# Performance work log

Hardware: AMD Instinct MI355X
Metric: run time of the kernel (lower is better)

The kernel has to match this reference:

```python
import jax, jax.numpy as jnp
import numpy as np

NCHW = ('NCHW', 'OIHW', 'NCHW')


def _conv3x3_same(x, w, b):
    # ZeroPad2d(1) + 3x3 valid conv == 3x3 conv with padding 1
    y = jax.lax.conv_general_dilated(x, w, window_strides=(1, 1),
                                     padding=((1, 1), (1, 1)),
                                     dimension_numbers=NCHW)
    return y + b[None, :, None, None]


def _maxpool2(x):
    return jax.lax.reduce_window(x, -jnp.inf, jax.lax.max,
                                 (1, 1, 2, 2), (1, 1, 2, 2), 'VALID')


def setup_inputs() -> dict:
    key = jax.random.key(0)
    ks = jax.random.split(key, 12)
    B, T1, T2, R, D = 1, 512, 512, 9, 3840
    q = jax.random.normal(ks[0], (B, T1, R, D), jnp.float32)
    t = jax.random.normal(ks[1], (B, T2, R, D), jnp.float32)
    # ViSiL features are L2-normalized region descriptors -> sims in [-1,1]
    q = q / jnp.linalg.norm(q, axis=-1, keepdims=True)
    t = t / jnp.linalg.norm(t, axis=-1, keepdims=True)
    s = 0.05
    return {
        'query': q, 'target': t,
        'w1': jax.random.normal(ks[2], (32, 1, 3, 3), jnp.float32) * s,
        'b1': jax.random.normal(ks[3], (32,), jnp.float32) * s,
        'w2': jax.random.normal(ks[4], (64, 32, 3, 3), jnp.float32) * s,
        'b2': jax.random.normal(ks[5], (64,), jnp.float32) * s,
        'w3': jax.random.normal(ks[6], (128, 64, 3, 3), jnp.float32) * s,
        'b3': jax.random.normal(ks[7], (128,), jnp.float32) * s,
        'wf': jax.random.normal(ks[8], (1, 128, 1, 1), jnp.float32) * s,
        'bf': jax.random.normal(ks[9], (1,), jnp.float32) * s,
    }


def reference(query, target, w1, b1, w2, b2, w3, b3, wf, bf):
    # frame-to-frame: region-pair similarity [B,T1,O,P,T2]
    sim5 = jnp.einsum('biok,bjpk->biopj', query, target)
    # Chamfer (axes=[3,2]): max over target regions P, mean over query regions O
    f2f = jnp.mean(jnp.max(sim5, axis=3), axis=2)  # [B,T1,T2]
    # video comperator CNN
    x = f2f[:, None]                                 # [B,1,T1,T2]
    x = _maxpool2(jax.nn.relu(_conv3x3_same(x, w1, b1)))
    x = _maxpool2(jax.nn.relu(_conv3x3_same(x, w2, b2)))
    x = jax.nn.relu(_conv3x3_same(x, w3, b3))
    x = jax.lax.conv_general_dilated(x, wf, (1, 1), ((0, 0), (0, 0)),
                                     dimension_numbers=NCHW)
    x = x + bf[None, :, None, None]
    s = jnp.clip(x[:, 0], -1.0, 1.0)                 # Hardtanh, [B,H,W]
    # video-to-video Chamfer (axes=[2,1]): max over axis 2, mean over axis 1
    return jnp.mean(jnp.max(s, axis=2), axis=1)      # [B]
```

## Files before the change

kernel.cpp:

```cpp
#include <hip/hip_runtime.h>
#include <hip/hip_bf16.h>

typedef float f32x4 __attribute__((ext_vector_type(4)));

#define AS3 __attribute__((address_space(3)))
#define AS1 __attribute__((address_space(1)))

__global__ __launch_bounds__(256) void cvt_fp8_kernel(const float* __restrict__ src,
                                                      unsigned int* __restrict__ dst,
                                                      int n16) {
  int idx = blockIdx.x * 256 + threadIdx.x;
  if (idx >= n16) return;
  const float4* s4 = (const float4*)src;
  uint4 o;
  unsigned int* op = (unsigned int*)&o;
#pragma unroll
  for (int i = 0; i < 4; ++i) {
    float4 v = s4[idx * 4 + i];
    int w = 0;
    w = __builtin_amdgcn_cvt_pk_fp8_f32(v.x * 16.f, v.y * 16.f, w, false);
    w = __builtin_amdgcn_cvt_pk_fp8_f32(v.z * 16.f, v.w * 16.f, w, true);
    op[i] = w;
  }
  ((uint4*)dst)[idx] = o;
}

__global__ __launch_bounds__(768) void gemm_cmax_kernel(const unsigned char* __restrict__ qf8,
                                                        const unsigned char* __restrict__ tf8,
                                                        float* __restrict__ cmax) {
  __shared__ __align__(16) char smem[73728];
  const int tid  = threadIdx.x;
  const int wv   = tid >> 6;
  const int lane = tid & 63;
  const int quad = lane >> 4;
  const int l16  = lane & 15;
  const int wrow = wv >> 1, wcol = wv & 1;
  const int bi = blockIdx.y, bj = blockIdx.x;

  f32x4 acc[3][9];
#pragma unroll
  for (int a = 0; a < 3; ++a)
#pragma unroll
    for (int b = 0; b < 9; ++b) acc[a][b] = (f32x4){0.f, 0.f, 0.f, 0.f};

  const unsigned char* gptr[3];
#pragma unroll
  for (int r = 0; r < 3; ++r) {
    int c   = r * 768 + wv * 64 + lane;
    int mat = (c >= 1152);
    int cm  = c - mat * 1152;
    int row = cm >> 2, cl = cm & 3;
    int gch = cl ^ ((row >> 1) & 3);
    const unsigned char* base = mat ? (tf8 + (size_t)(bj * 288 + row) * 3840)
                                    : (qf8 + (size_t)(bi * 288 + row) * 3840);
    gptr[r] = base + gch * 16;
  }

  int buf = 0;
#pragma unroll
  for (int r = 0; r < 3; ++r)
    __builtin_amdgcn_global_load_lds((const AS1 void*)(gptr[r]),
                                     (AS3 void*)(smem + (r * 768 + wv * 64) * 16), 16, 0, 0);

  const int arow0 = wrow * 48 + l16;
  const int bcol0 = wcol * 144 + l16;

  for (int kt = 0; kt < 60; ++kt) {
    __syncthreads();
    if (kt < 59) {
      int nb = buf ^ 1;
#pragma unroll
      for (int r = 0; r < 3; ++r)
        __builtin_amdgcn_global_load_lds((const AS1 void*)(gptr[r] + (kt + 1) * 64),
                                         (AS3 void*)(smem + nb * 36864 + (r * 768 + wv * 64) * 16),
                                         16, 0, 0);
    }
    const char* A = smem + buf * 36864;
    const char* B = A + 18432;
#pragma unroll
    for (int ks = 0; ks < 2; ++ks) {
      long av[3];
#pragma unroll
      for (int sr = 0; sr < 3; ++sr) {
        int row = arow0 + sr * 16;
        int ch  = ((ks * 2 + (quad >> 1)) ^ ((row >> 1) & 3));
        av[sr] = *(const long*)(A + row * 64 + ch * 16 + (quad & 1) * 8);
      }
#pragma unroll
      for (int c = 0; c < 9; ++c) {
        int col = bcol0 + c * 16;
        int ch  = ((ks * 2 + (quad >> 1)) ^ ((col >> 1) & 3));
        long bv = *(const long*)(B + col * 64 + ch * 16 + (quad & 1) * 8);
        acc[0][c] = __builtin_amdgcn_mfma_f32_16x16x32_fp8_fp8(av[0], bv, acc[0][c], 0, 0, 0);
        acc[1][c] = __builtin_amdgcn_mfma_f32_16x16x32_fp8_fp8(av[1], bv, acc[1][c], 0, 0, 0);
        acc[2][c] = __builtin_amdgcn_mfma_f32_16x16x32_fp8_fp8(av[2], bv, acc[2][c], 0, 0, 0);
      }
    }
    buf ^= 1;
  }

  __syncthreads();
  float* scr = (float*)smem;
#pragma unroll
  for (int b = 0; b < 18; ++b) {
    const int bw = b / 3, bs = b - bw * 3;
    if (wrow == bw) {
#pragma unroll
      for (int c = 0; c < 9; ++c)
#pragma unroll
        for (int r = 0; r < 4; ++r)
          scr[(quad * 4 + r) * 288 + wcol * 144 + c * 16 + l16] = acc[bs][c][r] * (1.f / 256.f);
    }
    __syncthreads();
    if (tid < 512) {
      int row = tid >> 5, jg = tid & 31;
      const float* p = scr + row * 288 + jg * 9;
      float m = p[0];
#pragma unroll
      for (int k = 1; k < 9; ++k) m = fmaxf(m, p[k]);
      cmax[(size_t)(bi * 288 + b * 16 + row) * 512 + bj * 32 + jg] = m;
    }
    __syncthreads();
  }
}

__global__ __launch_bounds__(512) void mean9_kernel(const float* __restrict__ cmax,
                                                    float* __restrict__ f2f) {
  int i = blockIdx.x, j = threadIdx.x;
  float s = 0.f;
#pragma unroll
  for (int o = 0; o < 9; ++o) s += cmax[(size_t)(i * 9 + o) * 512 + j];
  f2f[i * 512 + j] = s * (1.f / 9.f);
}

__global__ __launch_bounds__(256) void conv1_kernel(const float* __restrict__ in,
                                                    const float* __restrict__ w1,
                                                    const float* __restrict__ b1,
                                                    float* __restrict__ out) {
  __shared__ float tile[34 * 36];
  __shared__ float wl[320];
  int t = blockIdx.x;
  int ty0 = (t >> 4) * 32, tx0 = (t & 15) * 32;
  int py = threadIdx.x >> 4, px = threadIdx.x & 15;

  for (int idx = threadIdx.x; idx < 320; idx += 256)
    wl[idx] = (idx < 288) ? w1[idx] : b1[idx - 288];
  for (int idx = threadIdx.x; idx < 34 * 34; idx += 256) {
    int r = idx / 34, c = idx % 34;
    int gy = ty0 + r - 1, gx = tx0 + c - 1;
    tile[r * 36 + c] = ((unsigned)gy < 512u && (unsigned)gx < 512u) ? in[gy * 512 + gx] : 0.f;
  }
  __syncthreads();

  float win[4][4];
#pragma unroll
  for (int r = 0; r < 4; ++r)
#pragma unroll
    for (int c = 0; c < 4; ++c)
      win[r][c] = tile[(2 * py + r) * 36 + 2 * px + c];

  int gy2 = (t >> 4) * 16 + py, gx2 = (t & 15) * 16 + px;
#pragma unroll 1
  for (int ch = 0; ch < 32; ++ch) {
    float w[9];
#pragma unroll
    for (int k = 0; k < 9; ++k) w[k] = wl[ch * 9 + k];
    float m = -INFINITY;
#pragma unroll
    for (int a = 0; a < 2; ++a)
#pragma unroll
      for (int b = 0; b < 2; ++b) {
        float s = 0.f;
#pragma unroll
        for (int ky = 0; ky < 3; ++ky)
#pragma unroll
          for (int kx = 0; kx < 3; ++kx) s += win[a + ky][b + kx] * w[ky * 3 + kx];
        m = fmaxf(m, s);
      }
    out[ch * 65536 + gy2 * 256 + gx2] = fmaxf(m + wl[288 + ch], 0.f);
  }
}

__global__ __launch_bounds__(256) void conv2_kernel(const float* __restrict__ in,
                                                    const float* __restrict__ w2,
                                                    const float* __restrict__ b2,
                                                    float* __restrict__ out) {
  __shared__ __align__(16) float wlds[32 * 8 * 12];
  __shared__ float tile[2][2][34 * 36];
  const int tid = threadIdx.x;
  int cog = blockIdx.x >> 6;
  int t   = blockIdx.x & 63;
  int ty0 = (t >> 3) * 32, tx0 = (t & 7) * 32;
  int py = tid >> 4, px = tid & 15;

  for (int idx = tid; idx < 2304; idx += 256) {
    int co = idx / 288, rem = idx % 288, ci = rem / 9, k = rem % 9;
    wlds[(ci * 8 + co) * 12 + k] = w2[((cog * 8 + co) * 32 + ci) * 9 + k];
  }
  for (int idx = tid; idx < 2312; idx += 256) {
    int pl = idx / 1156, rc = idx % 1156, r = rc / 34, c = rc % 34;
    int gy = ty0 + r - 1, gx = tx0 + c - 1;
    tile[0][pl][r * 36 + c] = ((unsigned)gy < 256u && (unsigned)gx < 256u)
                                  ? in[pl * 65536 + gy * 256 + gx] : 0.f;
  }
  __syncthreads();

  float acc[4][8];
#pragma unroll
  for (int p = 0; p < 4; ++p)
#pragma unroll
    for (int co = 0; co < 8; ++co) acc[p][co] = 0.f;

#pragma unroll 1
  for (int cb = 0; cb < 16; ++cb) {
    int buf = cb & 1;
    float pf[10];
    if (cb < 15) {
#pragma unroll
      for (int i = 0; i < 10; ++i) {
        int idx = tid + i * 256;
        float v = 0.f;
        if (idx < 2312) {
          int pl = idx / 1156, rc = idx % 1156, r = rc / 34, c = rc % 34;
          int gy = ty0 + r - 1, gx = tx0 + c - 1;
          if ((unsigned)gy < 256u && (unsigned)gx < 256u)
            v = in[((cb + 1) * 2 + pl) * 65536 + gy * 256 + gx];
        }
        pf[i] = v;
      }
    }
#pragma unroll
    for (int pl = 0; pl < 2; ++pl) {
      float win[4][4];
#pragma unroll
      for (int r = 0; r < 4; ++r) {
        float2 lo = *(const float2*)&tile[buf][pl][(2 * py + r) * 36 + 2 * px];
        float2 hi = *(const float2*)&tile[buf][pl][(2 * py + r) * 36 + 2 * px + 2];
        win[r][0] = lo.x; win[r][1] = lo.y; win[r][2] = hi.x; win[r][3] = hi.y;
      }
      int ci = cb * 2 + pl;
#pragma unroll
      for (int co = 0; co < 8; ++co) {
        const float* wp = &wlds[(ci * 8 + co) * 12];
        float4 w0 = *(const float4*)wp;
        float4 w1v = *(const float4*)(wp + 4);
        float w8 = wp[8];
        float w[9] = {w0.x, w0.y, w0.z, w0.w, w1v.x, w1v.y, w1v.z, w1v.w, w8};
#pragma unroll
        for (int a = 0; a < 2; ++a)
#pragma unroll
          for (int b = 0; b < 2; ++b) {
            float s = acc[a * 2 + b][co];
#pragma unroll
            for (int ky = 0; ky < 3; ++ky)
#pragma unroll
              for (int kx = 0; kx < 3; ++kx) s += win[a + ky][b + kx] * w[ky * 3 + kx];
            acc[a * 2 + b][co] = s;
          }
      }
    }
    if (cb < 15) {
#pragma unroll
      for (int i = 0; i < 10; ++i) {
        int idx = tid + i * 256;
        if (idx < 2312) {
          int pl = idx / 1156, rc = idx % 1156, r = rc / 34, c = rc % 34;
          tile[buf ^ 1][pl][r * 36 + c] = pf[i];
        }
      }
    }
    __syncthreads();
  }

  int gy2 = (t >> 3) * 16 + py, gx2 = (t & 7) * 16 + px;
#pragma unroll
  for (int co = 0; co < 8; ++co) {
    float m = fmaxf(fmaxf(acc[0][co], acc[1][co]), fmaxf(acc[2][co], acc[3][co]));
    out[(cog * 8 + co) * 16384 + gy2 * 128 + gx2] = fmaxf(m + b2[cog * 8 + co], 0.f);
  }
}

__global__ __launch_bounds__(256) void conv3_kernel(const float* __restrict__ in,
                                                    const float* __restrict__ w3,
                                                    const float* __restrict__ b3,
                                                    float* __restrict__ out) {
  __shared__ __align__(16) float wlds[64 * 8 * 12];
  __shared__ float tile[2][4][18 * 40];
  const int tid = threadIdx.x;
  int cog = blockIdx.x >> 5;
  int t   = blockIdx.x & 31;
  int ty0 = (t >> 2) * 16, tx0 = (t & 3) * 32;
  int py = tid >> 4, px = tid & 15;

  for (int idx = tid; idx < 4608; idx += 256) {
    int co = idx / 576, rem = idx % 576, ci = rem / 9, k = rem % 9;
    wlds[(ci * 8 + co) * 12 + k] = w3[((cog * 8 + co) * 64 + ci) * 9 + k];
  }
  for (int idx = tid; idx < 2448; idx += 256) {
    int pl = idx / 612, rc = idx % 612, r = rc / 34, c = rc % 34;
    int gy = ty0 + r - 1, gx = tx0 + c - 1;
    tile[0][pl][r * 40 + c] = ((unsigned)gy < 128u && (unsigned)gx < 128u)
                                  ? in[pl * 16384 + gy * 128 + gx] : 0.f;
  }
  __syncthreads();

  float acc[2][8];
#pragma unroll
  for (int p = 0; p < 2; ++p)
#pragma unroll
    for (int co = 0; co < 8; ++co) acc[p][co] = 0.f;

#pragma unroll 1
  for (int cb = 0; cb < 16; ++cb) {
    int buf = cb & 1;
    float pf[10];
    if (cb < 15) {
#pragma unroll
      for (int i = 0; i < 10; ++i) {
        int idx = tid + i * 256;
        float v = 0.f;
        if (idx < 2448) {
          int pl = idx / 612, rc = idx % 612, r = rc / 34, c = rc % 34;
          int gy = ty0 + r - 1, gx = tx0 + c - 1;
          if ((unsigned)gy < 128u && (unsigned)gx < 128u)
            v = in[((cb + 1) * 4 + pl) * 16384 + gy * 128 + gx];
        }
        pf[i] = v;
      }
    }
#pragma unroll
    for (int pl = 0; pl < 4; ++pl) {
      float win[3][6];
#pragma unroll
      for (int r = 0; r < 3; ++r) {
#pragma unroll
        for (int c = 0; c < 3; ++c) {
          win[r][c]     = tile[buf][pl][(py + r) * 40 + px + c];
          win[r][3 + c] = tile[buf][pl][(py + r) * 40 + px + 16 + c];
        }
      }
      int ci = cb * 4 + pl;
#pragma unroll
      for (int co = 0; co < 8; ++co) {
        const float* wp = &wlds[(ci * 8 + co) * 12];
        float4 w0 = *(const float4*)wp;
        float4 w1v = *(const float4*)(wp + 4);
        float w8 = wp[8];
        float w[9] = {w0.x, w0.y, w0.z, w0.w, w1v.x, w1v.y, w1v.z, w1v.w, w8};
        float s0 = acc[0][co], s1 = acc[1][co];
#pragma unroll
        for (int ky = 0; ky < 3; ++ky)
#pragma unroll
          for (int kx = 0; kx < 3; ++kx) {
            s0 += win[ky][kx] * w[ky * 3 + kx];
            s1 += win[ky][3 + kx] * w[ky * 3 + kx];
          }
        acc[0][co] = s0; acc[1][co] = s1;
      }
    }
    if (cb < 15) {
#pragma unroll
      for (int i = 0; i < 10; ++i) {
        int idx = tid + i * 256;
        if (idx < 2448) {
          int pl = idx / 612, rc = idx % 612, r = rc / 34, c = rc % 34;
          tile[buf ^ 1][pl][r * 40 + c] = pf[i];
        }
      }
    }
    __syncthreads();
  }

  int y = ty0 + py;
#pragma unroll
  for (int co = 0; co < 8; ++co) {
    float bias = b3[cog * 8 + co];
    out[(cog * 8 + co) * 16384 + y * 128 + tx0 + px]      = fmaxf(acc[0][co] + bias, 0.f);
    out[(cog * 8 + co) * 16384 + y * 128 + tx0 + px + 16] = fmaxf(acc[1][co] + bias, 0.f);
  }
}

__global__ __launch_bounds__(512) void convf_kernel(const float* __restrict__ in,
                                                    const float* __restrict__ wf,
                                                    const float* __restrict__ bfp,
                                                    float* __restrict__ rowm) {
  __shared__ float part[512];
  int y = blockIdx.x, tid = threadIdx.x;
  int pt = tid >> 7, x = tid & 127;
  float acc = 0.f;
  const float* ip = in + y * 128 + x;
  for (int ci = pt * 32; ci < pt * 32 + 32; ++ci) acc += ip[ci * 16384] * wf[ci];
  part[tid] = acc;
  __syncthreads();
  if (tid < 128) {
    float s = part[tid] + part[tid + 128] + part[tid + 256] + part[tid + 384] + bfp[0];
    part[tid] = fminf(fmaxf(s, -1.f), 1.f);
  }
  __syncthreads();
  if (tid < 64) {
    float m = fmaxf(part[tid], part[tid + 64]);
    for (int off = 32; off; off >>= 1) m = fmaxf(m, __shfl_down(m, off, 64));
    if (tid == 0) rowm[y] = m;
  }
}

__global__ __launch_bounds__(128) void final_kernel(const float* __restrict__ rowm,
                                                    float* __restrict__ out) {
  int x = threadIdx.x;
  float v = rowm[x];
  for (int off = 32; off; off >>= 1) v += __shfl_down(v, off, 64);
  __shared__ float red[2];
  if ((x & 63) == 0) red[x >> 6] = v;
  __syncthreads();
  if (x == 0) out[0] = (red[0] + red[1]) * (1.f / 128.f);
}

extern "C" void kernel_launch(void* const* d_in, const int* in_sizes, int n_in,
                              void* d_out, int out_size, void* d_ws, size_t ws_size,
                              hipStream_t stream) {
  const float* q  = (const float*)d_in[0];
  const float* t  = (const float*)d_in[1];
  const float* w1 = (const float*)d_in[2];
  const float* b1 = (const float*)d_in[3];
  const float* w2 = (const float*)d_in[4];
  const float* b2 = (const float*)d_in[5];
  const float* w3 = (const float*)d_in[6];
  const float* b3 = (const float*)d_in[7];
  const float* wf = (const float*)d_in[8];
  const float* bf = (const float*)d_in[9];
  float* out = (float*)d_out;
  char* ws = (char*)d_ws;

  unsigned char* qf8 = (unsigned char*)(ws + 0);
  unsigned char* tf8 = (unsigned char*)(ws + 17694720);
  float* cmax = (float*)(ws + 35389440);
  float* f2f  = (float*)(ws + 44826624);
  float* x1   = (float*)(ws + 45875200);
  float* x2b  = (float*)(ws + 54263808);
  float* x3   = (float*)(ws + 58458112);
  float* rowm = (float*)(ws + 66846720);

  cvt_fp8_kernel<<<4320, 256, 0, stream>>>(q, (unsigned int*)qf8, 1105920);
  cvt_fp8_kernel<<<4320, 256, 0, stream>>>(t, (unsigned int*)tf8, 1105920);
  gemm_cmax_kernel<<<dim3(16, 16), 768, 0, stream>>>(qf8, tf8, cmax);
  mean9_kernel<<<512, 512, 0, stream>>>(cmax, f2f);
  conv1_kernel<<<256, 256, 0, stream>>>(f2f, w1, b1, x1);
  conv2_kernel<<<512, 256, 0, stream>>>(x1, w2, b2, x2b);
  conv3_kernel<<<512, 256, 0, stream>>>(x2b, w3, b3, x3);
  convf_kernel<<<128, 512, 0, stream>>>(x3, wf, bf, rowm);
  final_kernel<<<1, 128, 0, stream>>>(rowm, out);
}
```

Before: 461.1 us.

## Use 16x16x128 scaled FP8 MFMA in GEMM and retile conv2/conv3 blocks

The GEMM now loads 128-byte K slices per stage, using an 8-way XOR swizzle and 144KB of double-buffered LDS, and issues the MX-scaled 16x16x128 f8f6f4 MFMA with unit scales in place of 16x16x32 FP8. This halves the number of K iterations and barriers. conv2 now computes 4 output channels per block instead of 8, doubling the grid. conv3 switches to 32x32 tiles where each thread computes 2x2 pixels for 4 channels. The aim is more MFMA throughput and better occupancy for the conv stages, but the larger LDS footprint may limit the GEMM to one block per CU.

```diff
diff --git a/kernel.cpp b/kernel.cpp
--- a/kernel.cpp
+++ b/kernel.cpp
@@ -2,6 +2,7 @@
 #include <hip/hip_bf16.h>
 
 typedef float f32x4 __attribute__((ext_vector_type(4)));
+typedef int v8i __attribute__((ext_vector_type(8)));
 
 #define AS3 __attribute__((address_space(3)))
 #define AS1 __attribute__((address_space(1)))
@@ -28,7 +29,7 @@
 __global__ __launch_bounds__(768) void gemm_cmax_kernel(const unsigned char* __restrict__ qf8,
                                                         const unsigned char* __restrict__ tf8,
                                                         float* __restrict__ cmax) {
-  __shared__ __align__(16) char smem[73728];
+  __shared__ __align__(16) char smem[147456];
   const int tid  = threadIdx.x;
   const int wv   = tid >> 6;
   const int lane = tid & 63;
@@ -43,58 +44,70 @@
 #pragma unroll
     for (int b = 0; b < 9; ++b) acc[a][b] = (f32x4){0.f, 0.f, 0.f, 0.f};
 
-  const unsigned char* gptr[3];
-#pragma unroll
-  for (int r = 0; r < 3; ++r) {
-    int c   = r * 768 + wv * 64 + lane;
-    int mat = (c >= 1152);
-    int cm  = c - mat * 1152;
-    int row = cm >> 2, cl = cm & 3;
-    int gch = cl ^ ((row >> 1) & 3);
+  const unsigned char* gptr[6];
+#pragma unroll
+  for (int r = 0; r < 6; ++r) {
+    int s   = r * 768 + wv * 64 + lane;
+    int mat = (s >= 2304);
+    int sm  = s - mat * 2304;
+    int row = sm >> 3, pc = sm & 7;
+    int gc  = pc ^ (row & 7);
     const unsigned char* base = mat ? (tf8 + (size_t)(bj * 288 + row) * 3840)
                                     : (qf8 + (size_t)(bi * 288 + row) * 3840);
-    gptr[r] = base + gch * 16;
+    gptr[r] = base + gc * 16;
   }
 
   int buf = 0;
 #pragma unroll
-  for (int r = 0; r < 3; ++r)
+  for (int r = 0; r < 6; ++r)
     __builtin_amdgcn_global_load_lds((const AS1 void*)(gptr[r]),
                                      (AS3 void*)(smem + (r * 768 + wv * 64) * 16), 16, 0, 0);
 
   const int arow0 = wrow * 48 + l16;
   const int bcol0 = wcol * 144 + l16;
 
-  for (int kt = 0; kt < 60; ++kt) {
+  for (int kt = 0; kt < 30; ++kt) {
     __syncthreads();
-    if (kt < 59) {
+    if (kt < 29) {
       int nb = buf ^ 1;
 #pragma unroll
-      for (int r = 0; r < 3; ++r)
-        __builtin_amdgcn_global_load_lds((const AS1 void*)(gptr[r] + (kt + 1) * 64),
-                                         (AS3 void*)(smem + nb * 36864 + (r * 768 + wv * 64) * 16),
+      for (int r = 0; r < 6; ++r)
+        __builtin_amdgcn_global_load_lds((const AS1 void*)(gptr[r] + (kt + 1) * 128),
+                                         (AS3 void*)(smem + nb * 73728 + (r * 768 + wv * 64) * 16),
                                          16, 0, 0);
     }
-    const char* A = smem + buf * 36864;
-    const char* B = A + 18432;
-#pragma unroll
-    for (int ks = 0; ks < 2; ++ks) {
-      long av[3];
-#pragma unroll
-      for (int sr = 0; sr < 3; ++sr) {
-        int row = arow0 + sr * 16;
-        int ch  = ((ks * 2 + (quad >> 1)) ^ ((row >> 1) & 3));
-        av[sr] = *(const long*)(A + row * 64 + ch * 16 + (quad & 1) * 8);
-      }
-#pragma unroll
-      for (int c = 0; c < 9; ++c) {
-        int col = bcol0 + c * 16;
-        int ch  = ((ks * 2 + (quad >> 1)) ^ ((col >> 1) & 3));
-        long bv = *(const long*)(B + col * 64 + ch * 16 + (quad & 1) * 8);
-        acc[0][c] = __builtin_amdgcn_mfma_f32_16x16x32_fp8_fp8(av[0], bv, acc[0][c], 0, 0, 0);
-        acc[1][c] = __builtin_amdgcn_mfma_f32_16x16x32_fp8_fp8(av[1], bv, acc[1][c], 0, 0, 0);
-        acc[2][c] = __builtin_amdgcn_mfma_f32_16x16x32_fp8_fp8(av[2], bv, acc[2][c], 0, 0, 0);
-      }
+    const char* A = smem + buf * 73728;
+    const char* B = A + 36864;
+
+    v8i av[3];
+#pragma unroll
+    for (int sr = 0; sr < 3; ++sr) {
+      int row = arow0 + sr * 16;
+      int sw  = row & 7;
+      int p0  = (quad * 2) ^ sw, p1 = (quad * 2 + 1) ^ sw;
+      int4 lo = *(const int4*)(A + row * 128 + p0 * 16);
+      int4 hi = *(const int4*)(A + row * 128 + p1 * 16);
+      v8i v;
+      v[0] = lo.x; v[1] = lo.y; v[2] = lo.z; v[3] = lo.w;
+      v[4] = hi.x; v[5] = hi.y; v[6] = hi.z; v[7] = hi.w;
+      av[sr] = v;
+    }
+#pragma unroll
+    for (int c = 0; c < 9; ++c) {
+      int col = bcol0 + c * 16;
+      int sw  = col & 7;
+      int p0  = (quad * 2) ^ sw, p1 = (quad * 2 + 1) ^ sw;
+      int4 lo = *(const int4*)(B + col * 128 + p0 * 16);
+      int4 hi = *(const int4*)(B + col * 128 + p1 * 16);
+      v8i bv;
+      bv[0] = lo.x; bv[1] = lo.y; bv[2] = lo.z; bv[3] = lo.w;
+      bv[4] = hi.x; bv[5] = hi.y; bv[6] = hi.z; bv[7] = hi.w;
+      acc[0][c] = __builtin_amdgcn_mfma_scale_f32_16x16x128_f8f6f4(
+          av[0], bv, acc[0][c], 0, 0, 0, 0x7f7f7f7f, 0, 0x7f7f7f7f);
+      acc[1][c] = __builtin_amdgcn_mfma_scale_f32_16x16x128_f8f6f4(
+          av[1], bv, acc[1][c], 0, 0, 0, 0x7f7f7f7f, 0, 0x7f7f7f7f);
+      acc[2][c] = __builtin_amdgcn_mfma_scale_f32_16x16x128_f8f6f4(
+          av[2], bv, acc[2][c], 0, 0, 0, 0x7f7f7f7f, 0, 0x7f7f7f7f);
     }
     buf ^= 1;
   }
@@ -185,7 +198,7 @@
                                                     const float* __restrict__ w2,
                                                     const float* __restrict__ b2,
                                                     float* __restrict__ out) {
-  __shared__ __align__(16) float wlds[32 * 8 * 12];
+  __shared__ __align__(16) float wlds[32 * 4 * 12];
   __shared__ float tile[2][2][34 * 36];
   const int tid = threadIdx.x;
   int cog = blockIdx.x >> 6;
@@ -193,9 +206,9 @@
   int ty0 = (t >> 3) * 32, tx0 = (t & 7) * 32;
   int py = tid >> 4, px = tid & 15;
 
-  for (int idx = tid; idx < 2304; idx += 256) {
+  for (int idx = tid; idx < 1152; idx += 256) {
     int co = idx / 288, rem = idx % 288, ci = rem / 9, k = rem % 9;
-    wlds[(ci * 8 + co) * 12 + k] = w2[((cog * 8 + co) * 32 + ci) * 9 + k];
+    wlds[(ci * 4 + co) * 12 + k] = w2[((cog * 4 + co) * 32 + ci) * 9 + k];
   }
   for (int idx = tid; idx < 2312; idx += 256) {
     int pl = idx / 1156, rc = idx % 1156, r = rc / 34, c = rc % 34;
@@ -205,11 +218,11 @@
   }
   __syncthreads();
 
-  float acc[4][8];
+  float acc[4][4];
 #pragma unroll
   for (int p = 0; p < 4; ++p)
 #pragma unroll
-    for (int co = 0; co < 8; ++co) acc[p][co] = 0.f;
+    for (int co = 0; co < 4; ++co) acc[p][co] = 0.f;
 
 #pragma unroll 1
   for (int cb = 0; cb < 16; ++cb) {
@@ -240,8 +253,8 @@
       }
       int ci = cb * 2 + pl;
 #pragma unroll
-      for (int co = 0; co < 8; ++co) {
-        const float* wp = &wlds[(ci * 8 + co) * 12];
+      for (int co = 0; co < 4; ++co) {
+        const float* wp = &wlds[(ci * 4 + co) * 12];
         float4 w0 = *(const float4*)wp;
         float4 w1v = *(const float4*)(wp + 4);
         float w8 = wp[8];
@@ -274,9 +287,9 @@
 
   int gy2 = (t >> 3) * 16 + py, gx2 = (t & 7) * 16 + px;
 #pragma unroll
-  for (int co = 0; co < 8; ++co) {
+  for (int co = 0; co < 4; ++co) {
     float m = fmaxf(fmaxf(acc[0][co], acc[1][co]), fmaxf(acc[2][co], acc[3][co]));
-    out[(cog * 8 + co) * 16384 + gy2 * 128 + gx2] = fmaxf(m + b2[cog * 8 + co], 0.f);
+    out[(cog * 4 + co) * 16384 + gy2 * 128 + gx2] = fmaxf(m + b2[cog * 4 + co], 0.f);
   }
 }
 
@@ -284,43 +297,43 @@
                                                     const float* __restrict__ w3,
                                                     const float* __restrict__ b3,
                                                     float* __restrict__ out) {
-  __shared__ __align__(16) float wlds[64 * 8 * 12];
-  __shared__ float tile[2][4][18 * 40];
+  __shared__ __align__(16) float wlds[64 * 4 * 12];
+  __shared__ float tile[2][4][34 * 36];
   const int tid = threadIdx.x;
-  int cog = blockIdx.x >> 5;
-  int t   = blockIdx.x & 31;
-  int ty0 = (t >> 2) * 16, tx0 = (t & 3) * 32;
+  int cog = blockIdx.x >> 4;
+  int t   = blockIdx.x & 15;
+  int ty0 = (t >> 2) * 32, tx0 = (t & 3) * 32;
   int py = tid >> 4, px = tid & 15;
 
-  for (int idx = tid; idx < 4608; idx += 256) {
+  for (int idx = tid; idx < 2304; idx += 256) {
     int co = idx / 576, rem = idx % 576, ci = rem / 9, k = rem % 9;
-    wlds[(ci * 8 + co) * 12 + k] = w3[((cog * 8 + co) * 64 + ci) * 9 + k];
-  }
-  for (int idx = tid; idx < 2448; idx += 256) {
-    int pl = idx / 612, rc = idx % 612, r = rc / 34, c = rc % 34;
+    wlds[(ci * 4 + co) * 12 + k] = w3[((cog * 4 + co) * 64 + ci) * 9 + k];
+  }
+  for (int idx = tid; idx < 4624; idx += 256) {
+    int pl = idx / 1156, rc = idx % 1156, r = rc / 34, c = rc % 34;
     int gy = ty0 + r - 1, gx = tx0 + c - 1;
-    tile[0][pl][r * 40 + c] = ((unsigned)gy < 128u && (unsigned)gx < 128u)
+    tile[0][pl][r * 36 + c] = ((unsigned)gy < 128u && (unsigned)gx < 128u)
                                   ? in[pl * 16384 + gy * 128 + gx] : 0.f;
   }
   __syncthreads();
 
-  float acc[2][8];
-#pragma unroll
-  for (int p = 0; p < 2; ++p)
-#pragma unroll
-    for (int co = 0; co < 8; ++co) acc[p][co] = 0.f;
+  float acc[4][4];
+#pragma unroll
+  for (int p = 0; p < 4; ++p)
+#pragma unroll
+    for (int co = 0; co < 4; ++co) acc[p][co] = 0.f;
 
 #pragma unroll 1
   for (int cb = 0; cb < 16; ++cb) {
     int buf = cb & 1;
-    float pf[10];
+    float pf[19];
     if (cb < 15) {
 #pragma unroll
-      for (int i = 0; i < 10; ++i) {
+      for (int i = 0; i < 19; ++i) {
         int idx = tid + i * 256;
         float v = 0.f;
-        if (idx < 2448) {
-          int pl = idx / 612, rc = idx % 612, r = rc / 34, c = rc % 34;
+        if (idx < 4624) {
+          int pl = idx / 1156, rc = idx % 1156, r = rc / 34, c = rc % 34;
           int gy = ty0 + r - 1, gx = tx0 + c - 1;
           if ((unsigned)gy < 128u && (unsigned)gx < 128u)
             v = in[((cb + 1) * 4 + pl) * 16384 + gy * 128 + gx];
@@ -330,53 +343,56 @@
     }
 #pragma unroll
     for (int pl = 0; pl < 4; ++pl) {
-      float win[3][6];
-#pragma unroll
-      for (int r = 0; r < 3; ++r) {
-#pragma unroll
-        for (int c = 0; c < 3; ++c) {
-          win[r][c]     = tile[buf][pl][(py + r) * 40 + px + c];
-          win[r][3 + c] = tile[buf][pl][(py + r) * 40 + px + 16 + c];
-        }
+      float win[4][4];
+#pragma unroll
+      for (int r = 0; r < 4; ++r) {
+        float2 lo = *(const float2*)&tile[buf][pl][(2 * py + r) * 36 + 2 * px];
+        float2 hi = *(const float2*)&tile[buf][pl][(2 * py + r) * 36 + 2 * px + 2];
+        win[r][0] = lo.x; win[r][1] = lo.y; win[r][2] = hi.x; win[r][3] = hi.y;
       }
       int ci = cb * 4 + pl;
 #pragma unroll
-      for (int co = 0; co < 8; ++co) {
-        const float* wp = &wlds[(ci * 8 + co) * 12];
+      for (int co = 0; co < 4; ++co) {
+        const float* wp = &wlds[(ci * 4 + co) * 12];
         float4 w0 = *(const float4*)wp;
         float4 w1v = *(const float4*)(wp + 4);
         float w8 = wp[8];
         float w[9] = {w0.x, w0.y, w0.z, w0.w, w1v.x, w1v.y, w1v.z, w1v.w, w8};
-        float s0 = acc[0][co], s1 = acc[1][co];
-#pragma unroll
-        for (int ky = 0; ky < 3; ++ky)
-#pragma unroll
-          for (int kx = 0; kx < 3; ++kx) {
-            s0 += win[ky][kx] * w[ky * 3 + kx];
-            s1 += win[ky][3 + kx] * w[ky * 3 + kx];
+#pragma unroll
+        for (int a = 0; a < 2; ++a)
+#pragma unroll
+          for (int b = 0; b < 2; ++b) {
+            float s = acc[a * 2 + b][co];
+#pragma unroll
+            for (int ky = 0; ky < 3; ++ky)
+#pragma unroll
+              for (int kx = 0; kx < 3; ++kx) s += win[a + ky][b + kx] * w[ky * 3 + kx];
+            acc[a * 2 + b][co] = s;
           }
-        acc[0][co] = s0; acc[1][co] = s1;
       }
     }
     if (cb < 15) {
 #pragma unroll
-      for (int i = 0; i < 10; ++i) {
+      for (int i = 0; i < 19; ++i) {
         int idx = tid + i * 256;
-        if (idx < 2448) {
-          int pl = idx / 612, rc = idx % 612, r = rc / 34, c = rc % 34;
-          tile[buf ^ 1][pl][r * 40 + c] = pf[i];
+        if (idx < 4624) {
+          int pl = idx / 1156, rc = idx % 1156, r = rc / 34, c = rc % 34;
+          tile[buf ^ 1][pl][r * 36 + c] = pf[i];
         }
       }
     }
     __syncthreads();
   }
 
-  int y = ty0 + py;
-#pragma unroll
-  for (int co = 0; co < 8; ++co) {
-    float bias = b3[cog * 8 + co];
-    out[(cog * 8 + co) * 16384 + y * 128 + tx0 + px]      = fmaxf(acc[0][co] + bias, 0.f);
-    out[(cog * 8 + co) * 16384 + y * 128 + tx0 + px + 16] = fmaxf(acc[1][co] + bias, 0.f);
+#pragma unroll
+  for (int co = 0; co < 4; ++co) {
+    float bias = b3[cog * 4 + co];
+    float* op = out + (cog * 4 + co) * 16384;
+#pragma unroll
+    for (int a = 0; a < 2; ++a)
+#pragma unroll
+      for (int b = 0; b < 2; ++b)
+        op[(ty0 + 2 * py + a) * 128 + tx0 + 2 * px + b] = fmaxf(acc[a * 2 + b][co] + bias, 0.f);
   }
 }
 
@@ -445,7 +461,7 @@
   gemm_cmax_kernel<<<dim3(16, 16), 768, 0, stream>>>(qf8, tf8, cmax);
   mean9_kernel<<<512, 512, 0, stream>>>(cmax, f2f);
   conv1_kernel<<<256, 256, 0, stream>>>(f2f, w1, b1, x1);
-  conv2_kernel<<<512, 256, 0, stream>>>(x1, w2, b2, x2b);
+  conv2_kernel<<<1024, 256, 0, stream>>>(x1, w2, b2, x2b);
   conv3_kernel<<<512, 256, 0, stream>>>(x2b, w3, b3, x3);
   convf_kernel<<<128, 512, 0, stream>>>(x3, wf, bf, rowm);
   final_kernel<<<1, 128, 0, stream>>>(rowm, out);
```

After: 444.4 us. 1.04x faster.

## Switch GEMM to scaled 16x16x128 FP8 MFMA with K-major LDS layout, fuse conversions

Applied to the files above, without the earlier changes.

The FP8 GEMM now uses the MI355X mfma_scale 16x16x128 f8f6f4 instruction instead of 16x16x32. It doubles the K tile to 128 bytes per stage, which needs a 144KB double-buffered LDS with a K-chunk-major layout, and it remaps the block index to tile the grid for L2 locality. The two fp8 conversion launches are merged into one kernel. The conv2 and conv3 kernels now precompute global and LDS offsets once, which removes per-iteration div/mod. Conv3's tile row stride changes from 40 to 35. The larger LDS footprint limits occupancy to one block per CU, and the unit scale bytes must be correct for results to match.

```diff
diff --git a/kernel.cpp b/kernel.cpp
--- a/kernel.cpp
+++ b/kernel.cpp
@@ -2,15 +2,21 @@
 #include <hip/hip_bf16.h>
 
 typedef float f32x4 __attribute__((ext_vector_type(4)));
+typedef int v8i __attribute__((ext_vector_type(8)));
 
 #define AS3 __attribute__((address_space(3)))
 #define AS1 __attribute__((address_space(1)))
 
-__global__ __launch_bounds__(256) void cvt_fp8_kernel(const float* __restrict__ src,
-                                                      unsigned int* __restrict__ dst,
+__global__ __launch_bounds__(256) void cvt_fp8_kernel(const float* __restrict__ q,
+                                                      const float* __restrict__ t,
+                                                      unsigned int* __restrict__ qd,
+                                                      unsigned int* __restrict__ td,
                                                       int n16) {
   int idx = blockIdx.x * 256 + threadIdx.x;
-  if (idx >= n16) return;
+  const float* src;
+  unsigned int* dst;
+  if (idx < n16) { src = q; dst = qd; }
+  else           { idx -= n16; if (idx >= n16) return; src = t; dst = td; }
   const float4* s4 = (const float4*)src;
   uint4 o;
   unsigned int* op = (unsigned int*)&o;
@@ -28,14 +34,16 @@
 __global__ __launch_bounds__(768) void gemm_cmax_kernel(const unsigned char* __restrict__ qf8,
                                                         const unsigned char* __restrict__ tf8,
                                                         float* __restrict__ cmax) {
-  __shared__ __align__(16) char smem[73728];
+  __shared__ __align__(16) char smem[147456];
   const int tid  = threadIdx.x;
   const int wv   = tid >> 6;
   const int lane = tid & 63;
   const int quad = lane >> 4;
   const int l16  = lane & 15;
   const int wrow = wv >> 1, wcol = wv & 1;
-  const int bi = blockIdx.y, bj = blockIdx.x;
+  const int x = blockIdx.x & 7, r = blockIdx.x >> 3;
+  const int bi = (x >> 1) * 4 + (r & 3);
+  const int bj = (x & 1) * 8 + (r >> 2);
 
   f32x4 acc[3][9];
 #pragma unroll
@@ -43,58 +51,66 @@
 #pragma unroll
     for (int b = 0; b < 9; ++b) acc[a][b] = (f32x4){0.f, 0.f, 0.f, 0.f};
 
-  const unsigned char* gptr[3];
-#pragma unroll
-  for (int r = 0; r < 3; ++r) {
-    int c   = r * 768 + wv * 64 + lane;
-    int mat = (c >= 1152);
-    int cm  = c - mat * 1152;
-    int row = cm >> 2, cl = cm & 3;
-    int gch = cl ^ ((row >> 1) & 3);
+  const unsigned char* gptr[6];
+  int ldst[6];
+#pragma unroll
+  for (int i = 0; i < 6; ++i) {
+    int s   = i * 768 + tid;
+    int mat = (s >= 2304);
+    int sm  = s - mat * 2304;
+    int kc  = sm / 288, row = sm % 288;
     const unsigned char* base = mat ? (tf8 + (size_t)(bj * 288 + row) * 3840)
                                     : (qf8 + (size_t)(bi * 288 + row) * 3840);
-    gptr[r] = base + gch * 16;
+    gptr[i] = base + kc * 16;
+    ldst[i] = s * 16;
   }
 
   int buf = 0;
 #pragma unroll
-  for (int r = 0; r < 3; ++r)
-    __builtin_amdgcn_global_load_lds((const AS1 void*)(gptr[r]),
-                                     (AS3 void*)(smem + (r * 768 + wv * 64) * 16), 16, 0, 0);
-
-  const int arow0 = wrow * 48 + l16;
-  const int bcol0 = wcol * 144 + l16;
-
-  for (int kt = 0; kt < 60; ++kt) {
+  for (int i = 0; i < 6; ++i)
+    __builtin_amdgcn_global_load_lds((const AS1 void*)(gptr[i]),
+                                     (AS3 void*)(smem + ldst[i]), 16, 0, 0);
+
+  const int arow = wrow * 48 + l16;
+  const int bcol = wcol * 144 + l16;
+
+  for (int kt = 0; kt < 30; ++kt) {
     __syncthreads();
-    if (kt < 59) {
+    if (kt < 29) {
       int nb = buf ^ 1;
 #pragma unroll
-      for (int r = 0; r < 3; ++r)
-        __builtin_amdgcn_global_load_lds((const AS1 void*)(gptr[r] + (kt + 1) * 64),
-                                         (AS3 void*)(smem + nb * 36864 + (r * 768 + wv * 64) * 16),
-                                         16, 0, 0);
-    }
-    const char* A = smem + buf * 36864;
-    const char* B = A + 18432;
-#pragma unroll
-    for (int ks = 0; ks < 2; ++ks) {
-      long av[3];
-#pragma unroll
-      for (int sr = 0; sr < 3; ++sr) {
-        int row = arow0 + sr * 16;
-        int ch  = ((ks * 2 + (quad >> 1)) ^ ((row >> 1) & 3));
-        av[sr] = *(const long*)(A + row * 64 + ch * 16 + (quad & 1) * 8);
-      }
-#pragma unroll
-      for (int c = 0; c < 9; ++c) {
-        int col = bcol0 + c * 16;
-        int ch  = ((ks * 2 + (quad >> 1)) ^ ((col >> 1) & 3));
-        long bv = *(const long*)(B + col * 64 + ch * 16 + (quad & 1) * 8);
-        acc[0][c] = __builtin_amdgcn_mfma_f32_16x16x32_fp8_fp8(av[0], bv, acc[0][c], 0, 0, 0);
-        acc[1][c] = __builtin_amdgcn_mfma_f32_16x16x32_fp8_fp8(av[1], bv, acc[1][c], 0, 0, 0);
-        acc[2][c] = __builtin_amdgcn_mfma_f32_16x16x32_fp8_fp8(av[2], bv, acc[2][c], 0, 0, 0);
-      }
+      for (int i = 0; i < 6; ++i)
+        __builtin_amdgcn_global_load_lds((const AS1 void*)(gptr[i] + (kt + 1) * 128),
+                                         (AS3 void*)(smem + nb * 73728 + ldst[i]), 16, 0, 0);
+    }
+    const char* A = smem + buf * 73728;
+    const char* B = A + 36864;
+
+    v8i av[3];
+#pragma unroll
+    for (int sr = 0; sr < 3; ++sr) {
+      int rr = arow + sr * 16;
+      int4 lo = *(const int4*)(A + ((quad * 2) * 288 + rr) * 16);
+      int4 hi = *(const int4*)(A + ((quad * 2 + 1) * 288 + rr) * 16);
+      v8i v;
+      v[0] = lo.x; v[1] = lo.y; v[2] = lo.z; v[3] = lo.w;
+      v[4] = hi.x; v[5] = hi.y; v[6] = hi.z; v[7] = hi.w;
+      av[sr] = v;
+    }
+#pragma unroll
+    for (int c = 0; c < 9; ++c) {
+      int cc = bcol + c * 16;
+      int4 lo = *(const int4*)(B + ((quad * 2) * 288 + cc) * 16);
+      int4 hi = *(const int4*)(B + ((quad * 2 + 1) * 288 + cc) * 16);
+      v8i bv;
+      bv[0] = lo.x; bv[1] = lo.y; bv[2] = lo.z; bv[3] = lo.w;
+      bv[4] = hi.x; bv[5] = hi.y; bv[6] = hi.z; bv[7] = hi.w;
+      acc[0][c] = __builtin_amdgcn_mfma_scale_f32_16x16x128_f8f6f4(
+          av[0], bv, acc[0][c], 0, 0, 0, 0x7f7f7f7f, 0, 0x7f7f7f7f);
+      acc[1][c] = __builtin_amdgcn_mfma_scale_f32_16x16x128_f8f6f4(
+          av[1], bv, acc[1][c], 0, 0, 0, 0x7f7f7f7f, 0, 0x7f7f7f7f);
+      acc[2][c] = __builtin_amdgcn_mfma_scale_f32_16x16x128_f8f6f4(
+          av[2], bv, acc[2][c], 0, 0, 0, 0x7f7f7f7f, 0, 0x7f7f7f7f);
     }
     buf ^= 1;
   }
@@ -108,8 +124,8 @@
 #pragma unroll
       for (int c = 0; c < 9; ++c)
 #pragma unroll
-        for (int r = 0; r < 4; ++r)
-          scr[(quad * 4 + r) * 288 + wcol * 144 + c * 16 + l16] = acc[bs][c][r] * (1.f / 256.f);
+        for (int rr = 0; rr < 4; ++rr)
+          scr[(quad * 4 + rr) * 288 + wcol * 144 + c * 16 + l16] = acc[bs][c][rr] * (1.f / 256.f);
     }
     __syncthreads();
     if (tid < 512) {
@@ -186,7 +202,7 @@
                                                     const float* __restrict__ b2,
                                                     float* __restrict__ out) {
   __shared__ __align__(16) float wlds[32 * 8 * 12];
-  __shared__ float tile[2][2][34 * 36];
+  __shared__ float tile[2 * 2448];
   const int tid = threadIdx.x;
   int cog = blockIdx.x >> 6;
   int t   = blockIdx.x & 63;
@@ -197,12 +213,20 @@
     int co = idx / 288, rem = idx % 288, ci = rem / 9, k = rem % 9;
     wlds[(ci * 8 + co) * 12 + k] = w2[((cog * 8 + co) * 32 + ci) * 9 + k];
   }
-  for (int idx = tid; idx < 2312; idx += 256) {
-    int pl = idx / 1156, rc = idx % 1156, r = rc / 34, c = rc % 34;
-    int gy = ty0 + r - 1, gx = tx0 + c - 1;
-    tile[0][pl][r * 36 + c] = ((unsigned)gy < 256u && (unsigned)gx < 256u)
-                                  ? in[pl * 65536 + gy * 256 + gx] : 0.f;
-  }
+  int goffs[10], loffs[10];
+#pragma unroll
+  for (int i = 0; i < 10; ++i) {
+    int idx = tid + i * 256;
+    if (idx < 2312) {
+      int pl = idx / 1156, rc = idx % 1156, rr = rc / 34, cc = rc % 34;
+      loffs[i] = pl * 1224 + rr * 36 + cc;
+      int gy = ty0 + rr - 1, gx = tx0 + cc - 1;
+      goffs[i] = ((unsigned)gy < 256u && (unsigned)gx < 256u) ? pl * 65536 + gy * 256 + gx : -1;
+    } else { loffs[i] = -1; goffs[i] = -1; }
+  }
+#pragma unroll
+  for (int i = 0; i < 10; ++i)
+    if (loffs[i] >= 0) tile[loffs[i]] = (goffs[i] >= 0) ? in[goffs[i]] : 0.f;
   __syncthreads();
 
   float acc[4][8];
@@ -217,26 +241,18 @@
     float pf[10];
     if (cb < 15) {
 #pragma unroll
-      for (int i = 0; i < 10; ++i) {
-        int idx = tid + i * 256;
-        float v = 0.f;
-        if (idx < 2312) {
-          int pl = idx / 1156, rc = idx % 1156, r = rc / 34, c = rc % 34;
-          int gy = ty0 + r - 1, gx = tx0 + c - 1;
-          if ((unsigned)gy < 256u && (unsigned)gx < 256u)
-            v = in[((cb + 1) * 2 + pl) * 65536 + gy * 256 + gx];
-        }
-        pf[i] = v;
-      }
-    }
+      for (int i = 0; i < 10; ++i)
+        pf[i] = (goffs[i] >= 0) ? in[goffs[i] + (cb + 1) * 131072] : 0.f;
+    }
+    const float* tb = tile + buf * 2448;
 #pragma unroll
     for (int pl = 0; pl < 2; ++pl) {
       float win[4][4];
 #pragma unroll
-      for (int r = 0; r < 4; ++r) {
-        float2 lo = *(const float2*)&tile[buf][pl][(2 * py + r) * 36 + 2 * px];
-        float2 hi = *(const float2*)&tile[buf][pl][(2 * py + r) * 36 + 2 * px + 2];
-        win[r][0] = lo.x; win[r][1] = lo.y; win[r][2] = hi.x; win[r][3] = hi.y;
+      for (int rr = 0; rr < 4; ++rr) {
+        float2 lo = *(const float2*)&tb[pl * 1224 + (2 * py + rr) * 36 + 2 * px];
+        float2 hi = *(const float2*)&tb[pl * 1224 + (2 * py + rr) * 36 + 2 * px + 2];
+        win[rr][0] = lo.x; win[rr][1] = lo.y; win[rr][2] = hi.x; win[rr][3] = hi.y;
       }
       int ci = cb * 2 + pl;
 #pragma unroll
@@ -261,13 +277,8 @@
     }
     if (cb < 15) {
 #pragma unroll
-      for (int i = 0; i < 10; ++i) {
-        int idx = tid + i * 256;
-        if (idx < 2312) {
-          int pl = idx / 1156, rc = idx % 1156, r = rc / 34, c = rc % 34;
-          tile[buf ^ 1][pl][r * 36 + c] = pf[i];
-        }
-      }
+      for (int i = 0; i < 10; ++i)
+        if (loffs[i] >= 0) tile[(buf ^ 1) * 2448 + loffs[i]] = pf[i];
     }
     __syncthreads();
   }
@@ -285,7 +296,7 @@
                                                     const float* __restrict__ b3,
                                                     float* __restrict__ out) {
   __shared__ __align__(16) float wlds[64 * 8 * 12];
-  __shared__ float tile[2][4][18 * 40];
+  __shared__ float tile[2 * 2520];
   const int tid = threadIdx.x;
   int cog = blockIdx.x >> 5;
   int t   = blockIdx.x & 31;
@@ -296,19 +307,25 @@
     int co = idx / 576, rem = idx % 576, ci = rem / 9, k = rem % 9;
     wlds[(ci * 8 + co) * 12 + k] = w3[((cog * 8 + co) * 64 + ci) * 9 + k];
   }
-  for (int idx = tid; idx < 2448; idx += 256) {
-    int pl = idx / 612, rc = idx % 612, r = rc / 34, c = rc % 34;
-    int gy = ty0 + r - 1, gx = tx0 + c - 1;
-    tile[0][pl][r * 40 + c] = ((unsigned)gy < 128u && (unsigned)gx < 128u)
-                                  ? in[pl * 16384 + gy * 128 + gx] : 0.f;
-  }
-  __syncthreads();
-
-  float acc[2][8];
-#pragma unroll
-  for (int p = 0; p < 2; ++p)
-#pragma unroll
-    for (int co = 0; co < 8; ++co) acc[p][co] = 0.f;
+  int goffs[10], loffs[10];
+#pragma unroll
+  for (int i = 0; i < 10; ++i) {
+    int idx = tid + i * 256;
+    if (idx < 2448) {
+      int pl = idx / 612, rc = idx % 612, rr = rc / 34, cc = rc % 34;
+      loffs[i] = pl * 630 + rr * 35 + cc;
+      int gy = ty0 + rr - 1, gx = tx0 + cc - 1;
+      goffs[i] = ((unsigned)gy < 128u && (unsigned)gx < 128u) ? pl * 16384 + gy * 128 + gx : -1;
+    } else { loffs[i] = -1; goffs[i] = -1; }
+  }
+#pragma unroll
+  for (int i = 0; i < 10; ++i)
+    if (loffs[i] >= 0) tile[loffs[i]] = (goffs[i] >= 0) ? in[goffs[i]] : 0.f;
+  __syncthreads();
+
+  float acc0[8], acc1[8];
+#pragma unroll
+  for (int co = 0; co < 8; ++co) { acc0[co] = 0.f; acc1[co] = 0.f; }
 
 #pragma unroll 1
   for (int cb = 0; cb < 16; ++cb) {
@@ -316,29 +333,20 @@
     float pf[10];
     if (cb < 15) {
 #pragma unroll
-      for (int i = 0; i < 10; ++i) {
-        int idx = tid + i * 256;
-        float v = 0.f;
-        if (idx < 2448) {
-          int pl = idx / 612, rc = idx % 612, r = rc / 34, c = rc % 34;
-          int gy = ty0 + r - 1, gx = tx0 + c - 1;
-          if ((unsigned)gy < 128u && (unsigned)gx < 128u)
-            v = in[((cb + 1) * 4 + pl) * 16384 + gy * 128 + gx];
+      for (int i = 0; i < 10; ++i)
+        pf[i] = (goffs[i] >= 0) ? in[goffs[i] + (cb + 1) * 65536] : 0.f;
+    }
+    const float* tb = tile + buf * 2520;
+#pragma unroll
+    for (int pl = 0; pl < 4; ++pl) {
+      float wn[3][6];
+#pragma unroll
+      for (int rr = 0; rr < 3; ++rr)
+#pragma unroll
+        for (int cc = 0; cc < 3; ++cc) {
+          wn[rr][cc]     = tb[pl * 630 + (py + rr) * 35 + px + cc];
+          wn[rr][3 + cc] = tb[pl * 630 + (py + rr) * 35 + px + 16 + cc];
         }
-        pf[i] = v;
-      }
-    }
-#pragma unroll
-    for (int pl = 0; pl < 4; ++pl) {
-      float win[3][6];
-#pragma unroll
-      for (int r = 0; r < 3; ++r) {
-#pragma unroll
-        for (int c = 0; c < 3; ++c) {
-          win[r][c]     = tile[buf][pl][(py + r) * 40 + px + c];
-          win[r][3 + c] = tile[buf][pl][(py + r) * 40 + px + 16 + c];
-        }
-      }
       int ci = cb * 4 + pl;
 #pragma unroll
       for (int co = 0; co < 8; ++co) {
@@ -347,26 +355,21 @@
         float4 w1v = *(const float4*)(wp + 4);
         float w8 = wp[8];
         float w[9] = {w0.x, w0.y, w0.z, w0.w, w1v.x, w1v.y, w1v.z, w1v.w, w8};
-        float s0 = acc[0][co], s1 = acc[1][co];
+        float s0 = acc0[co], s1 = acc1[co];
 #pragma unroll
         for (int ky = 0; ky < 3; ++ky)
 #pragma unroll
           for (int kx = 0; kx < 3; ++kx) {
-            s0 += win[ky][kx] * w[ky * 3 + kx];
-            s1 += win[ky][3 + kx] * w[ky * 3 + kx];
+            s0 += wn[ky][kx] * w[ky * 3 + kx];
+            s1 += wn[ky][3 + kx] * w[ky * 3 + kx];
           }
-        acc[0][co] = s0; acc[1][co] = s1;
+        acc0[co] = s0; acc1[co] = s1;
       }
     }
     if (cb < 15) {
 #pragma unroll
-      for (int i = 0; i < 10; ++i) {
-        int idx = tid + i * 256;
-        if (idx < 2448) {
-          int pl = idx / 612, rc = idx % 612, r = rc / 34, c = rc % 34;
-          tile[buf ^ 1][pl][r * 40 + c] = pf[i];
-        }
-      }
+      for (int i = 0; i < 10; ++i)
+        if (loffs[i] >= 0) tile[(buf ^ 1) * 2520 + loffs[i]] = pf[i];
     }
     __syncthreads();
   }
@@ -375,8 +378,9 @@
 #pragma unroll
   for (int co = 0; co < 8; ++co) {
     float bias = b3[cog * 8 + co];
-    out[(cog * 8 + co) * 16384 + y * 128 + tx0 + px]      = fmaxf(acc[0][co] + bias, 0.f);
-    out[(cog * 8 + co) * 16384 + y * 128 + tx0 + px + 16] = fmaxf(acc[1][co] + bias, 0.f);
+    float* op = out + (cog * 8 + co) * 16384 + y * 128 + tx0 + px;
+    op[0]  = fmaxf(acc0[co] + bias, 0.f);
+    op[16] = fmaxf(acc1[co] + bias, 0.f);
   }
 }
 
@@ -440,9 +444,8 @@
   float* x3   = (float*)(ws + 58458112);
   float* rowm = (float*)(ws + 66846720);
 
-  cvt_fp8_kernel<<<4320, 256, 0, stream>>>(q, (unsigned int*)qf8, 1105920);
-  cvt_fp8_kernel<<<4320, 256, 0, stream>>>(t, (unsigned int*)tf8, 1105920);
-  gemm_cmax_kernel<<<dim3(16, 16), 768, 0, stream>>>(qf8, tf8, cmax);
+  cvt_fp8_kernel<<<8640, 256, 0, stream>>>(q, t, (unsigned int*)qf8, (unsigned int*)tf8, 1105920);
+  gemm_cmax_kernel<<<256, 768, 0, stream>>>(qf8, tf8, cmax);
   mean9_kernel<<<512, 512, 0, stream>>>(cmax, f2f);
   conv1_kernel<<<256, 256, 0, stream>>>(f2f, w1, b1, x1);
   conv2_kernel<<<512, 256, 0, stream>>>(x1, w2, b2, x2b);
```

After: 536.4 us. 1.16x slower.
